# Kernel tuning notes

Measured on AMD Instinct MI355X. Metric: run time of the kernel, lower is better.

The kernel has to match this reference:

```python
import jax, jax.numpy as jnp
import numpy as np

N = 50000       # nodes
E = 1_600_000   # edges (avg degree 32)
IN = 256        # in_dim
HID = 64        # hidden_dim
HEADS = 2
CLS = 10
NEG_SLOPE = 0.2  # PyG GATConv default leaky_relu slope


def gat_layer(x, edge_index, W, att_src, att_dst, bias, heads, concat):
    """PyG-style GATConv (eval mode, add_self_loops=True).
    x: [N, F_in]; W: [F_in, heads*C]; att_src/att_dst: [heads, C]; bias: [heads*C] or [C].
    """
    n = x.shape[0]
    loop = jnp.arange(n)
    src = jnp.concatenate([edge_index[0], loop])   # message sources j
    dst = jnp.concatenate([edge_index[1], loop])   # message targets i
    C = W.shape[1] // heads
    h = (x @ W).reshape(n, heads, C)               # [N, H, C]
    a_s = jnp.sum(h * att_src, axis=-1)            # [N, H]
    a_d = jnp.sum(h * att_dst, axis=-1)            # [N, H]
    e = jax.nn.leaky_relu(a_s[src] + a_d[dst], NEG_SLOPE)   # [E', H]
    # segment softmax over incoming edges of each destination node
    m = jax.lax.stop_gradient(jax.ops.segment_max(e, dst, num_segments=n))
    ex = jnp.exp(e - m[dst])
    denom = jax.ops.segment_sum(ex, dst, num_segments=n)
    alpha = ex / denom[dst]                         # [E', H]
    out = jax.ops.segment_sum(alpha[:, :, None] * h[src], dst, num_segments=n)  # [N, H, C]
    out = out.reshape(n, heads * C) if concat else out.mean(axis=1)
    return out + bias


def setup_inputs() -> dict:
    key = jax.random.key(0)
    ks = jax.random.split(key, 12)
    sd = lambda f: np.float32(1.0 / np.sqrt(f))
    x = jax.random.normal(ks[0], (N, IN), dtype=jnp.float32)
    edge_index = jax.random.randint(ks[1], (2, E), 0, N, dtype=jnp.int64)
    # layer 1: in_dim -> hidden, heads=2, concat
    W1 = jax.random.normal(ks[2], (IN, HEADS * HID), dtype=jnp.float32) * sd(IN)
    as1 = jax.random.normal(ks[3], (HEADS, HID), dtype=jnp.float32) * sd(HID)
    ad1 = jax.random.normal(ks[4], (HEADS, HID), dtype=jnp.float32) * sd(HID)
    b1 = jnp.zeros((HEADS * HID,), dtype=jnp.float32)
    # layer 2: hidden*heads -> hidden, heads=1, concat=False
    W2 = jax.random.normal(ks[5], (HEADS * HID, HID), dtype=jnp.float32) * sd(HEADS * HID)
    as2 = jax.random.normal(ks[6], (1, HID), dtype=jnp.float32) * sd(HID)
    ad2 = jax.random.normal(ks[7], (1, HID), dtype=jnp.float32) * sd(HID)
    b2 = jnp.zeros((HID,), dtype=jnp.float32)
    # linear head
    Wl = jax.random.normal(ks[8], (HID, CLS), dtype=jnp.float32) * sd(HID)
    bl = jnp.zeros((CLS,), dtype=jnp.float32)
    return {"x": x, "edge_index": edge_index,
            "W1": W1, "as1": as1, "ad1": ad1, "b1": b1,
            "W2": W2, "as2": as2, "ad2": ad2, "b2": b2,
            "Wl": Wl, "bl": bl}


def reference(x, edge_index, W1, as1, ad1, b1, W2, as2, ad2, b2, Wl, bl):
    h = jax.nn.elu(gat_layer(x, edge_index, W1, as1, ad1, b1, HEADS, True))
    h = jax.nn.elu(gat_layer(h, edge_index, W2, as2, ad2, b2, 1, False))
    return h @ Wl + bl  # [N, num_classes]
```

## Files before the change

### kernel.cpp

```cpp
#include <hip/hip_runtime.h>

#define NN 50000
#define NE 1600000
#define EP (NE + NN)
#define IN_DIM 256
#define HIDD 64
#define NCLS 10
#define NBKT 196
#define EPB 8192
#define NPB ((EP + EPB - 1) / EPB)
#define BCAP 12288

typedef unsigned short u16;
typedef short bf16x8 __attribute__((ext_vector_type(8)));
typedef float f32x4 __attribute__((ext_vector_type(4)));

__device__ __forceinline__ float b2f(u16 v) { return __uint_as_float(((unsigned)v) << 16); }
__device__ __forceinline__ u16 f2b(float f) {
    unsigned u = __float_as_uint(f);
    unsigned r = (u + 0x7FFFu + ((u >> 16) & 1u)) >> 16;
    return (u16)r;
}

__device__ __forceinline__ void load_edge(const int* __restrict__ ei, int m, int g,
                                          int& s, int& d) {
    if (g < NE) {
        if (m) { s = ei[2 * (size_t)g]; d = ei[2 * ((size_t)NE + g)]; }
        else   { s = ei[g];             d = ei[NE + g]; }
    } else {
        s = d = g - NE;
    }
    s = s < 0 ? 0 : (s >= NN ? NN - 1 : s);
    d = d < 0 ? 0 : (d >= NN ? NN - 1 : d);
}

__device__ __forceinline__ void wcvt_att_job(
    const float* __restrict__ W, const float* __restrict__ as,
    const float* __restrict__ ad, int K, int N, int H, u16* __restrict__ Wt,
    int idx) {
    if (idx >= K * (N + 16)) return;
    int n = idx / K, k = idx - n * K;
    if (n < N) { Wt[idx] = f2b(W[(size_t)k * N + n]); return; }
    int j = n - N;
    if (j >= 2 * H) { Wt[idx] = 0; return; }
    const float* att = (j & 1) ? ad : as;
    int h = j >> 1, C = N / H;
    float sum = 0.f;
    for (int c = 0; c < C; ++c)
        sum += W[(size_t)k * N + h * C + c] * att[h * C + c];
    Wt[idx] = f2b(sum);
}

__global__ __launch_bounds__(1024) void partition_k(
    const int* __restrict__ ei, int* __restrict__ gcursor,
    unsigned* __restrict__ bbuf,
    const float* __restrict__ W1, const float* __restrict__ as1,
    const float* __restrict__ ad1, u16* __restrict__ w1t,
    const float* __restrict__ W2, const float* __restrict__ as2,
    const float* __restrict__ ad2, u16* __restrict__ w2t,
    const float* __restrict__ Wl, u16* __restrict__ wlt) {
    __shared__ int hist[NBKT], base[NBKT], cur[NBKT];
    __shared__ unsigned stash[EPB];
    __shared__ int smode;
    int t = threadIdx.x, b = blockIdx.x;
    if (b < 36) wcvt_att_job(W1, as1, ad1, 256, 128, 2, w1t, b * 1024 + t);
    else if (b < 46) wcvt_att_job(W2, as2, ad2, 128, 64, 1, w2t, (b - 36) * 1024 + t);
    else if (b == 46) {
        int n = t >> 6, k = t & 63;
        wlt[n * 64 + k] = (n < NCLS) ? f2b(Wl[k * NCLS + n]) : (u16)0;
    }
    if (t < 64) {
        int nz = 0;
#pragma unroll
        for (int k = 0; k < 4; ++k)
            if (ei[2 * (t * 4 + k) + 1] != 0) nz = 1;
        unsigned long long bal = __ballot(nz);
        if (t == 0) smode = (bal == 0ULL) ? 1 : 0;
    }
    for (int i = t; i < NBKT; i += 1024) hist[i] = 0;
    __syncthreads();
    int m = smode;
    int g0 = b * EPB;
    int gend = min(g0 + EPB, EP);
    for (int g = g0 + t; g < gend; g += 1024) {
        int s, d;
        load_edge(ei, m, g, s, d);
        stash[g - g0] = ((unsigned)s << 16) | (unsigned)d;
        atomicAdd(&hist[d >> 8], 1);
    }
    __syncthreads();
    for (int i = t; i < NBKT; i += 1024) {
        base[i] = hist[i] ? atomicAdd(&gcursor[i], hist[i]) : 0;
        cur[i] = 0;
    }
    __syncthreads();
    int cnt = gend - g0;
    for (int l = t; l < cnt; l += 1024) {
        unsigned p = stash[l];
        int d = p & 0xFFFF;
        int bb = d >> 8;
        int r = base[bb] + atomicAdd(&cur[bb], 1);
        if (r < BCAP)
            bbuf[(size_t)bb * BCAP + r] = ((p >> 16) << 8) | (unsigned)(d & 255);
    }
}

__global__ __launch_bounds__(1024) void bucket_csr_k(const unsigned* __restrict__ bbuf,
                                                     const int* __restrict__ gcursor,
                                                     int* __restrict__ row_ptr,
                                                     u16* __restrict__ csr_src) {
    __shared__ int bsc[256];
    __shared__ int hist[256], scn[256], cur[256];
    __shared__ int se0, scnt, stot;
    int b = blockIdx.x, t = threadIdx.x;
    int v = 0;
    if (t < 256) {
        v = (t < NBKT) ? min(gcursor[t], BCAP) : 0;
        bsc[t] = v;
        hist[t] = 0;
    }
    __syncthreads();
    for (int off = 1; off < 256; off <<= 1) {
        int x = (t < 256 && t >= off) ? bsc[t - off] : 0;
        __syncthreads();
        if (t < 256) bsc[t] += x;
        __syncthreads();
    }
    if (t == b) { se0 = bsc[t] - v; scnt = v; }
    if (t == NBKT - 1) stot = bsc[t];
    __syncthreads();
    int e0 = se0, cnt = scnt;
    const unsigned* bb = bbuf + (size_t)b * BCAP;
    for (int e = t; e < cnt; e += 1024)
        atomicAdd(&hist[bb[e] & 255], 1);
    __syncthreads();
    int hv = 0;
    if (t < 256) { hv = hist[t]; scn[t] = hv; }
    __syncthreads();
    for (int off = 1; off < 256; off <<= 1) {
        int x = (t < 256 && t >= off) ? scn[t - off] : 0;
        __syncthreads();
        if (t < 256) scn[t] += x;
        __syncthreads();
    }
    if (t < 256) {
        int ex = scn[t] - hv;
        int n = b * 256 + t;
        if (n < NN) row_ptr[n] = e0 + ex;
        cur[t] = e0 + ex;
    }
    __syncthreads();
    for (int e = t; e < cnt; e += 1024) {
        unsigned p = bb[e];
        int pos = atomicAdd(&cur[p & 255], 1);
        csr_src[pos] = (u16)(p >> 8);
    }
    if (b == 0 && t == 0) row_ptr[NN] = stot;
}

template <int K, int NF, int H, bool F32A, bool SLICED_A>
__global__ __launch_bounds__(256) void gemm_mfma_att_k(
    const float* __restrict__ Af, const u16* __restrict__ Ab,
    const u16* __restrict__ Wt, u16* __restrict__ C,
    float* __restrict__ a_s, float* __restrict__ a_d) {
    constexpr int NTF = NF / 16, NT = NTF + 1, KS = K / 32;
    const int wave = threadIdx.x >> 6, lane = threadIdx.x & 63;
    const int quad = lane >> 4, l15 = lane & 15;
    const int m0 = blockIdx.x * 64 + wave * 16;
    int rowA = m0 + l15;
    if (rowA >= NN) rowA = NN - 1;
    const float* afp = F32A ? (Af + (size_t)rowA * K + quad * 8) : nullptr;
    const u16* abp = nullptr;
    if constexpr (!F32A) {
        abp = SLICED_A ? (Ab + (size_t)rowA * 32 + quad * 8)
                       : (Ab + (size_t)rowA * K + quad * 8);
    }
    const u16* bptr = Wt + (size_t)l15 * K + quad * 8;
    f32x4 acc[NT] = {};
#pragma unroll
    for (int ks = 0; ks < KS; ++ks) {
        bf16x8 af;
        if constexpr (F32A) {
            float4 v0 = *(const float4*)(afp + ks * 32);
            float4 v1 = *(const float4*)(afp + ks * 32 + 4);
            af[0] = (short)f2b(v0.x); af[1] = (short)f2b(v0.y);
            af[2] = (short)f2b(v0.z); af[3] = (short)f2b(v0.w);
            af[4] = (short)f2b(v1.x); af[5] = (short)f2b(v1.y);
            af[6] = (short)f2b(v1.z); af[7] = (short)f2b(v1.w);
        } else {
            af = SLICED_A ? *(const bf16x8*)(abp + (size_t)ks * (NN * 32))
                          : *(const bf16x8*)(abp + ks * 32);
        }
        bf16x8 bf[NT];
#pragma unroll
        for (int nt = 0; nt < NT; ++nt)
            bf[nt] = *(const bf16x8*)(bptr + (size_t)nt * 16 * K + ks * 32);
#pragma unroll
        for (int nt = 0; nt < NT; ++nt)
            acc[nt] = __builtin_amdgcn_mfma_f32_16x16x32_bf16(af, bf[nt], acc[nt], 0, 0, 0);
    }
#pragma unroll
    for (int nt = 0; nt < NTF; ++nt) {
#pragma unroll
        for (int reg = 0; reg < 4; ++reg) {
            int row = m0 + quad * 4 + reg;
            int c = nt * 16 + l15;
            if (row < NN)
                C[(size_t)(c >> 5) * (NN * 32) + (size_t)row * 32 + (c & 31)] =
                    f2b(acc[nt][reg]);
        }
    }
    if (l15 < 2 * H) {
        int h = l15 >> 1;
        float* dst = (l15 & 1) ? a_d : a_s;
#pragma unroll
        for (int reg = 0; reg < 4; ++reg) {
            int row = m0 + quad * 4 + reg;
            if (row < NN) dst[row * H + h] = acc[NTF][reg];
        }
    }
}

__global__ __launch_bounds__(256) void edge_alpha_k(
    const int* __restrict__ row_ptr, const u16* __restrict__ csr_src,
    const float* __restrict__ a_s, const float* __restrict__ a_d,
    unsigned* __restrict__ A2, float* __restrict__ dninv) {
    int wave = threadIdx.x >> 6;
    int pair = blockIdx.x * 4 + wave;
    if (pair >= NN / 2) return;
    int lane = threadIdx.x & 63, half = lane >> 5, hl = lane & 31;
    int node = pair * 2 + half;
    int r0 = row_ptr[node], r1 = row_ptr[node + 1];
    int cnt = r1 - r0;
    int co = max(cnt, __shfl_xor(cnt, 32));
    int nbat = (co + 31) >> 5;
    float adn = a_d[node];
    float dh = 0.f;
    for (int b = 0; b < nbat; ++b) {
        int idx = r0 + b * 32 + hl;
        bool act = idx < r1;
        int sl = act ? (int)csr_src[idx] : 0;
        float e = a_s[sl] + adn;
        e = e > 0.f ? e : 0.2f * e;
        e = fminf(e, 60.f);
        float ex = act ? __expf(e) : 0.f;
        dh += ex;
        if (act)
            __builtin_nontemporal_store(
                (unsigned)sl | ((unsigned)f2b(ex) << 16), A2 + idx);
    }
#pragma unroll
    for (int off = 1; off < 32; off <<= 1) dh += __shfl_xor(dh, off);
    if (hl == 0) dninv[node] = 1.0f / dh;
}

template <int CH, int NSL, int H, bool USE_EX>
__global__ __launch_bounds__(256) void gat_slice_k(
    const int* __restrict__ row_ptr, const u16* __restrict__ csr_src,
    const unsigned* __restrict__ A2, const float* __restrict__ a_s,
    const float* __restrict__ a_d, const float* __restrict__ dninv,
    const u16* __restrict__ h, const float* __restrict__ bias,
    u16* __restrict__ outg) {
    constexpr int SC = CH / NSL;
    constexpr int SUB = 8 / NSL;
    int xcd = blockIdx.x & 7;
    int slice = xcd / SUB;
    int sub = xcd % SUB;
    int pg = (blockIdx.x >> 3) * SUB + sub;
    int wave = threadIdx.x >> 6;
    int pair = pg * 4 + wave;
    if (pair >= NN / 2) return;
    int lane = threadIdx.x & 63;
    int half = lane >> 5, hl = lane & 31, q = hl & 7, gh = hl >> 3;
    int node = pair * 2 + half;
    int r0 = row_ptr[node], r1 = row_ptr[node + 1];
    int cnt = r1 - r0;
    int co = max(cnt, __shfl_xor(cnt, 32));
    int nbat = (co + 31) >> 5;
    const unsigned char* hb8 =
        (const unsigned char*)h + (size_t)slice * (NN * 64);
    const int head = (H == 2) ? (slice >> 1) : 0;
    float adn = 0.f, rdn = 0.f;
    if constexpr (USE_EX) rdn = dninv[node];
    else adn = a_d[node * H + head];
    float dh = 0.f;
    float acc[4] = {0.f, 0.f, 0.f, 0.f};
    const int abase = ((half << 5) | gh) << 2;
    for (int b = 0; b < nbat; ++b) {
        int idx = r0 + b * 32 + hl;
        bool act = idx < r1;
        unsigned pex;
        if constexpr (USE_EX) {
            pex = act ? __builtin_nontemporal_load(A2 + idx) : 0u;
        } else {
            int sl = act ? (int)__builtin_nontemporal_load(csr_src + idx) : 0;
            float e = a_s[sl * H + head] + adn;
            e = e > 0.f ? e : 0.2f * e;
            e = fminf(e, 60.f);
            float ex = act ? __expf(e) : 0.f;
            dh += ex;
            pex = (unsigned)sl | ((unsigned)f2b(ex) << 16);
        }
#pragma unroll
        for (int jr = 0; jr < 2; ++jr) {
            int pr[4];
#pragma unroll
            for (int i = 0; i < 4; ++i)
                pr[i] = __builtin_amdgcn_ds_bpermute(
                    abase + ((jr * 16 + i * 4) << 2), (int)pex);
            unsigned hv0[4], hv1[4];
#pragma unroll
            for (int i = 0; i < 4; ++i) {
                const unsigned* p = (const unsigned*)(
                    hb8 + (((unsigned)((unsigned)pr[i] & 0xFFFFu) << 6) + q * 8));
                hv0[i] = p[0];
                hv1[i] = p[1];
            }
#pragma unroll
            for (int i = 0; i < 4; ++i) {
                float exf = __uint_as_float((unsigned)pr[i] & 0xFFFF0000u);
                unsigned w0 = hv0[i], w1 = hv1[i];
                acc[0] += exf * __uint_as_float(w0 << 16);
                acc[1] += exf * __uint_as_float(w0 & 0xFFFF0000u);
                acc[2] += exf * __uint_as_float(w1 << 16);
                acc[3] += exf * __uint_as_float(w1 & 0xFFFF0000u);
            }
        }
    }
    if constexpr (!USE_EX) {
#pragma unroll
        for (int off = 1; off < 32; off <<= 1) dh += __shfl_xor(dh, off);
        rdn = 1.0f / dh;
    }
#pragma unroll
    for (int v = 0; v < 4; ++v) {
        acc[v] += __shfl_xor(acc[v], 8);
        acc[v] += __shfl_xor(acc[v], 16);
    }
    if (gh == 0) {
        float vv[4];
#pragma unroll
        for (int k = 0; k < 4; ++k) {
            float t = acc[k] * rdn + bias[slice * SC + q * 4 + k];
            vv[k] = t > 0.f ? t : expm1f(t);
        }
        unsigned long long ov =
            (unsigned long long)((unsigned)f2b(vv[0]) | ((unsigned)f2b(vv[1]) << 16)) |
            ((unsigned long long)((unsigned)f2b(vv[2]) | ((unsigned)f2b(vv[3]) << 16)) << 32);
        __builtin_nontemporal_store(
            ov, (unsigned long long*)(outg + (size_t)slice * (NN * 32) +
                                      (size_t)node * 32 + q * 4));
    }
}

__global__ __launch_bounds__(256) void head_gemm_k(
    const u16* __restrict__ A, const u16* __restrict__ Wt,
    const float* __restrict__ bl, float* __restrict__ out) {
    const int wave = threadIdx.x >> 6, lane = threadIdx.x & 63;
    const int quad = lane >> 4, l15 = lane & 15;
    const int m0 = blockIdx.x * 64 + wave * 16;
    int rowA = m0 + l15;
    if (rowA >= NN) rowA = NN - 1;
    const u16* ab = A + (size_t)rowA * 32 + quad * 8;
    const u16* bp = Wt + (size_t)l15 * 64 + quad * 8;
    f32x4 acc = {};
#pragma unroll
    for (int ks = 0; ks < 2; ++ks) {
        bf16x8 af = *(const bf16x8*)(ab + (size_t)ks * (NN * 32));
        bf16x8 bf = *(const bf16x8*)(bp + ks * 32);
        acc = __builtin_amdgcn_mfma_f32_16x16x32_bf16(af, bf, acc, 0, 0, 0);
    }
    if (l15 < NCLS) {
        float blv = bl[l15];
#pragma unroll
        for (int reg = 0; reg < 4; ++reg) {
            int row = m0 + quad * 4 + reg;
            if (row < NN) out[(size_t)row * NCLS + l15] = acc[reg] + blv;
        }
    }
}

extern "C" void kernel_launch(void* const* d_in, const int* in_sizes, int n_in,
                              void* d_out, int out_size, void* d_ws, size_t ws_size,
                              hipStream_t stream) {
    const float* x   = (const float*)d_in[0];
    const int*   ei  = (const int*)d_in[1];
    const float* W1  = (const float*)d_in[2];
    const float* as1 = (const float*)d_in[3];
    const float* ad1 = (const float*)d_in[4];
    const float* b1  = (const float*)d_in[5];
    const float* W2  = (const float*)d_in[6];
    const float* as2 = (const float*)d_in[7];
    const float* ad2 = (const float*)d_in[8];
    const float* b2  = (const float*)d_in[9];
    const float* Wl  = (const float*)d_in[10];
    const float* bl  = (const float*)d_in[11];
    float* out = (float*)d_out;

    float* ws = (float*)d_ws;
    size_t o = 0;
    u16* hb  = (u16*)(ws + o); o += (size_t)NN * 64;
    u16* g2  = hb + (size_t)NN * 64;
    u16* g1  = (u16*)(ws + o); o += (size_t)NN * 64;
    unsigned* bbuf = (unsigned*)g1;
    unsigned* A2 = (unsigned*)g1;
    float* dn2inv = (float*)((char*)g1 + (size_t)EP * 4);
    u16* w1t = (u16*)(ws + o); o += 144 * 256 / 2;
    u16* w2t = (u16*)(ws + o); o += 80 * 128 / 2;
    u16* wlt = (u16*)(ws + o); o += 16 * 64 / 2;
    float* a_s = ws + o;       o += (size_t)NN * 2;
    float* a_d = ws + o;       o += (size_t)NN * 2;
    int* ints = (int*)(ws + o);
    size_t io = 0;
    int* gcursor  = ints + io; io += NBKT;
    int* row_ptr  = ints + io; io += NN + 1;
    u16* csr_src  = (u16*)(ints + io); io += (EP + 1) / 2;

    hipMemsetAsync(gcursor, 0, NBKT * sizeof(int), stream);
    partition_k<<<NPB, 1024, 0, stream>>>(ei, gcursor, bbuf,
                                          W1, as1, ad1, w1t, W2, as2, ad2, w2t,
                                          Wl, wlt);
    bucket_csr_k<<<NBKT, 1024, 0, stream>>>(bbuf, gcursor, row_ptr, csr_src);

    const int gemmBlocks = (NN + 63) / 64;

    gemm_mfma_att_k<256, 128, 2, true, false><<<gemmBlocks, 256, 0, stream>>>(
        x, nullptr, w1t, hb, a_s, a_d);
    gat_slice_k<128, 4, 2, false><<<25000, 256, 0, stream>>>(
        row_ptr, csr_src, nullptr, a_s, a_d, nullptr, hb, b1, g1);

    gemm_mfma_att_k<128, 64, 1, false, true><<<gemmBlocks, 256, 0, stream>>>(
        nullptr, g1, w2t, hb, a_s, a_d);
    edge_alpha_k<<<(NN / 2 + 3) / 4, 256, 0, stream>>>(
        row_ptr, csr_src, a_s, a_d, A2, dn2inv);
    gat_slice_k<64, 2, 1, true><<<12504, 256, 0, stream>>>(
        row_ptr, csr_src, A2, nullptr, nullptr, dn2inv, hb, b2, g2);

    head_gemm_k<<<gemmBlocks, 256, 0, stream>>>(g2, wlt, bl, out);
}
```

Before: 350.0 us.

## Replace layer-1 sliced aggregation with wave-per-node gather kernel and local bucket sort

```diff
diff --git a/kernel.cpp b/kernel.cpp
--- a/kernel.cpp
+++ b/kernel.cpp
@@ -59,8 +59,9 @@
     const float* __restrict__ W2, const float* __restrict__ as2,
     const float* __restrict__ ad2, u16* __restrict__ w2t,
     const float* __restrict__ Wl, u16* __restrict__ wlt) {
-    __shared__ int hist[NBKT], base[NBKT], cur[NBKT];
-    __shared__ unsigned stash[EPB];
+    __shared__ int hist[NBKT], base[NBKT], lbase[NBKT], lcur[NBKT];
+    __shared__ int psc[256];
+    __shared__ unsigned sst[EPB];
     __shared__ int smode;
     int t = threadIdx.x, b = blockIdx.x;
     if (b < 36) wcvt_att_job(W1, as1, ad1, 256, 128, 2, w1t, b * 1024 + t);
@@ -85,23 +86,40 @@
     for (int g = g0 + t; g < gend; g += 1024) {
         int s, d;
         load_edge(ei, m, g, s, d);
-        stash[g - g0] = ((unsigned)s << 16) | (unsigned)d;
         atomicAdd(&hist[d >> 8], 1);
     }
     __syncthreads();
-    for (int i = t; i < NBKT; i += 1024) {
-        base[i] = hist[i] ? atomicAdd(&gcursor[i], hist[i]) : 0;
-        cur[i] = 0;
+    int hv = 0;
+    if (t < 256) { hv = (t < NBKT) ? hist[t] : 0; psc[t] = hv; }
+    __syncthreads();
+    for (int off = 1; off < 256; off <<= 1) {
+        int x = (t < 256 && t >= off) ? psc[t - off] : 0;
+        __syncthreads();
+        if (t < 256) psc[t] += x;
+        __syncthreads();
+    }
+    if (t < NBKT) {
+        lbase[t] = psc[t] - hv;
+        lcur[t] = 0;
+        base[t] = hv ? atomicAdd(&gcursor[t], hv) : 0;
+    }
+    __syncthreads();
+    for (int g = g0 + t; g < gend; g += 1024) {
+        int s, d;
+        load_edge(ei, m, g, s, d);
+        unsigned p = ((unsigned)s << 16) | (unsigned)d;
+        int bb = d >> 8;
+        int r = lbase[bb] + atomicAdd(&lcur[bb], 1);
+        sst[r] = p;
     }
     __syncthreads();
     int cnt = gend - g0;
     for (int l = t; l < cnt; l += 1024) {
-        unsigned p = stash[l];
-        int d = p & 0xFFFF;
-        int bb = d >> 8;
-        int r = base[bb] + atomicAdd(&cur[bb], 1);
-        if (r < BCAP)
-            bbuf[(size_t)bb * BCAP + r] = ((p >> 16) << 8) | (unsigned)(d & 255);
+        unsigned p = sst[l];
+        int bb = (p & 0xFFFF) >> 8;
+        int gp = base[bb] + (l - lbase[bb]);
+        if (gp < BCAP)
+            bbuf[(size_t)bb * BCAP + gp] = ((p >> 16) << 8) | (p & 255u);
     }
 }
 
@@ -112,6 +130,7 @@
     __shared__ int bsc[256];
     __shared__ int hist[256], scn[256], cur[256];
     __shared__ int se0, scnt, stot;
+    __shared__ u16 srt[BCAP];
     int b = blockIdx.x, t = threadIdx.x;
     int v = 0;
     if (t < 256) {
@@ -147,18 +166,21 @@
         int ex = scn[t] - hv;
         int n = b * 256 + t;
         if (n < NN) row_ptr[n] = e0 + ex;
-        cur[t] = e0 + ex;
+        cur[t] = ex;
     }
     __syncthreads();
     for (int e = t; e < cnt; e += 1024) {
         unsigned p = bb[e];
         int pos = atomicAdd(&cur[p & 255], 1);
-        csr_src[pos] = (u16)(p >> 8);
-    }
+        srt[pos] = (u16)(p >> 8);
+    }
+    __syncthreads();
+    for (int e = t; e < cnt; e += 1024)
+        csr_src[e0 + e] = srt[e];
     if (b == 0 && t == 0) row_ptr[NN] = stot;
 }
 
-template <int K, int NF, int H, bool F32A, bool SLICED_A>
+template <int K, int NF, int H, bool F32A, bool SLICED_A, bool SLICED_C>
 __global__ __launch_bounds__(256) void gemm_mfma_att_k(
     const float* __restrict__ Af, const u16* __restrict__ Ab,
     const u16* __restrict__ Wt, u16* __restrict__ C,
@@ -205,9 +227,13 @@
         for (int reg = 0; reg < 4; ++reg) {
             int row = m0 + quad * 4 + reg;
             int c = nt * 16 + l15;
-            if (row < NN)
-                C[(size_t)(c >> 5) * (NN * 32) + (size_t)row * 32 + (c & 31)] =
-                    f2b(acc[nt][reg]);
+            if (row < NN) {
+                if constexpr (SLICED_C)
+                    C[(size_t)(c >> 5) * (NN * 32) + (size_t)row * 32 + (c & 31)] =
+                        f2b(acc[nt][reg]);
+                else
+                    C[(size_t)row * NF + c] = f2b(acc[nt][reg]);
+            }
         }
     }
     if (l15 < 2 * H) {
@@ -217,6 +243,133 @@
         for (int reg = 0; reg < 4; ++reg) {
             int row = m0 + quad * 4 + reg;
             if (row < NN) dst[row * H + h] = acc[NTF][reg];
+        }
+    }
+}
+
+template <int CH, int H, bool HEAD>
+__global__ __launch_bounds__(256) void gat_gather_k(
+    const int* __restrict__ row_ptr, const u16* __restrict__ csr_src,
+    const float* __restrict__ a_s, const float* __restrict__ a_d,
+    const u16* __restrict__ h, const float* __restrict__ bias,
+    u16* __restrict__ outg, const float* __restrict__ Wl,
+    const float* __restrict__ bl, float* __restrict__ outh) {
+    constexpr int VEC = CH / 64;
+    constexpr int JB = 16;
+    int n = (blockIdx.x * blockDim.x + threadIdx.x) >> 6;
+    int lane = threadIdx.x & 63;
+    if (n >= NN) return;
+    int r0 = row_ptr[n], r1 = row_ptr[n + 1];
+    const bool hi = (VEC == 2) ? (lane >= 32) : false;
+    const int shl16 = hi ? 0 : 16;
+
+    float adn0, adn1 = 0.f;
+    if (H == 2) {
+        float2 adv = *(const float2*)(a_d + n * 2);
+        adn0 = adv.x; adn1 = adv.y;
+    } else {
+        adn0 = a_d[n];
+    }
+
+    float dh0 = 0.f, dh1 = 0.f;
+    float acc[VEC];
+#pragma unroll
+    for (int v = 0; v < VEC; ++v) acc[v] = 0.f;
+
+    for (int base = r0; base < r1; base += 64) {
+        int cnt = min(64, r1 - base);
+        int idx = base + lane;
+        bool act = idx < r1;
+        int sl = act ? (int)csr_src[idx] : 0;
+        unsigned pex;
+        if (H == 2) {
+            float2 av = *(const float2*)(a_s + sl * 2);
+            float e0 = av.x + adn0;
+            e0 = e0 > 0.f ? e0 : 0.2f * e0;
+            e0 = fminf(e0, 60.f);
+            float ex0 = act ? __expf(e0) : 0.f;
+            dh0 += ex0;
+            float e1 = av.y + adn1;
+            e1 = e1 > 0.f ? e1 : 0.2f * e1;
+            e1 = fminf(e1, 60.f);
+            float ex1 = act ? __expf(e1) : 0.f;
+            dh1 += ex1;
+            pex = (unsigned)f2b(ex0) | ((unsigned)f2b(ex1) << 16);
+        } else {
+            float e0 = a_s[sl] + adn0;
+            e0 = e0 > 0.f ? e0 : 0.2f * e0;
+            e0 = fminf(e0, 60.f);
+            float ex0 = act ? __expf(e0) : 0.f;
+            dh0 += ex0;
+            pex = (unsigned)sl | ((unsigned)f2b(ex0) << 16);
+        }
+        for (int j0 = 0; j0 < cnt; j0 += JB) {
+            if (VEC == 2) {
+                int ssu[JB];
+                unsigned peu[JB];
+#pragma unroll
+                for (int i = 0; i < JB; ++i) {
+                    ssu[i] = __builtin_amdgcn_readlane(sl, j0 + i);
+                    peu[i] = (unsigned)__builtin_amdgcn_readlane((int)pex, j0 + i);
+                }
+                unsigned hv[JB];
+#pragma unroll
+                for (int i = 0; i < JB; ++i)
+                    hv[i] = ((const unsigned*)(h + (size_t)ssu[i] * CH))[lane];
+#pragma unroll
+                for (int i = 0; i < JB; ++i) {
+                    float exv = __uint_as_float((peu[i] << shl16) & 0xFFFF0000u);
+                    acc[0] += exv * __uint_as_float(hv[i] << 16);
+                    acc[1] += exv * __uint_as_float(hv[i] & 0xFFFF0000u);
+                }
+            } else {
+                unsigned peu[JB];
+#pragma unroll
+                for (int i = 0; i < JB; ++i)
+                    peu[i] = (unsigned)__builtin_amdgcn_readlane((int)pex, j0 + i);
+                u16 hv[JB];
+#pragma unroll
+                for (int i = 0; i < JB; ++i)
+                    hv[i] = (h + (size_t)(peu[i] & 0xFFFFu) * CH)[lane];
+#pragma unroll
+                for (int i = 0; i < JB; ++i)
+                    acc[0] += __uint_as_float(peu[i] & 0xFFFF0000u) * b2f(hv[i]);
+            }
+        }
+    }
+
+#pragma unroll
+    for (int off = 32; off; off >>= 1) dh0 += __shfl_xor(dh0, off);
+    float dn = dh0;
+    if (H == 2) {
+#pragma unroll
+        for (int off = 32; off; off >>= 1) dh1 += __shfl_xor(dh1, off);
+        dn = hi ? dh1 : dh0;
+    }
+
+    if (VEC == 2) {
+        int c = lane * 2;
+        float2 bv = *(const float2*)(bias + c);
+        float v0 = acc[0] / dn + bv.x;
+        float v1 = acc[1] / dn + bv.y;
+        v0 = v0 > 0.f ? v0 : expm1f(v0);
+        v1 = v1 > 0.f ? v1 : expm1f(v1);
+        ushort2 ov;
+        ov.x = f2b(v0); ov.y = f2b(v1);
+        *(ushort2*)(outg + (size_t)(c >> 5) * (NN * 32) + (size_t)n * 32 + (c & 31)) = ov;
+    } else {
+        float v0 = acc[0] / dn + bias[lane];
+        v0 = v0 > 0.f ? v0 : expm1f(v0);
+        if (HEAD) {
+#pragma unroll
+            for (int cls = 0; cls < NCLS; ++cls) {
+                float p = v0 * Wl[lane * NCLS + cls];
+#pragma unroll
+                for (int off = 32; off; off >>= 1) p += __shfl_xor(p, off);
+                if (lane == cls) outh[(size_t)n * NCLS + cls] = p + bl[cls];
+            }
+        } else {
+            outg[(size_t)n * CH + lane] = f2b(v0);
         }
     }
 }
@@ -423,13 +576,14 @@
     bucket_csr_k<<<NBKT, 1024, 0, stream>>>(bbuf, gcursor, row_ptr, csr_src);
 
     const int gemmBlocks = (NN + 63) / 64;
-
-    gemm_mfma_att_k<256, 128, 2, true, false><<<gemmBlocks, 256, 0, stream>>>(
+    const int gatherBlocks = (NN + 3) / 4;
+
+    gemm_mfma_att_k<256, 128, 2, true, false, false><<<gemmBlocks, 256, 0, stream>>>(
         x, nullptr, w1t, hb, a_s, a_d);
-    gat_slice_k<128, 4, 2, false><<<25000, 256, 0, stream>>>(
-        row_ptr, csr_src, nullptr, a_s, a_d, nullptr, hb, b1, g1);
-
-    gemm_mfma_att_k<128, 64, 1, false, true><<<gemmBlocks, 256, 0, stream>>>(
+    gat_gather_k<128, 2, false><<<gatherBlocks, 256, 0, stream>>>(
+        row_ptr, csr_src, a_s, a_d, hb, b1, g1, nullptr, nullptr, nullptr);
+
+    gemm_mfma_att_k<128, 64, 1, false, true, true><<<gemmBlocks, 256, 0, stream>>>(
         nullptr, g1, w2t, hb, a_s, a_d);
     edge_alpha_k<<<(NN / 2 + 3) / 4, 256, 0, stream>>>(
         row_ptr, csr_src, a_s, a_d, A2, dn2inv);
```

New measurement: 304.2 us (median of 2 runs). 13.1% less time.
